# Kernel tuning notes

Measured on AMD Instinct MI355X. Metric: run time of the kernel, lower is better.

The kernel has to match this reference:

```python
import jax, jax.numpy as jnp
import numpy as np
import math

B, NI, NU, D, H, MAXNB, T = 1024, 50000, 20000, 256, 4, 20, 1000


def _cosine_sqrt_ab():
    t = jnp.linspace(0.0, T, T + 1) / T
    ab = jnp.cos((t + 0.008) / 1.008 * math.pi / 2) ** 2
    ab = ab / ab[0]
    ab = ab[1:]
    return jnp.sqrt(ab), jnp.sqrt(1.0 - ab)


def _ln(x, g, b, eps=1e-5):
    m = jnp.mean(x, -1, keepdims=True)
    v = jnp.var(x, -1, keepdims=True)
    return (x - m) / jnp.sqrt(v + eps) * g + b


def _mha(q, k, v, wqkv, bqkv, wo, bo):
    # torch nn.MultiheadAttention (batch_first) with packed in_proj
    d = q.shape[-1]
    dh = d // H
    wq, wk, wv = jnp.split(wqkv, 3, axis=0)
    bq, bk, bv = jnp.split(bqkv, 3, axis=0)
    def heads(x, w, bb):
        y = x @ w.T + bb
        return y.reshape(x.shape[0], x.shape[1], H, dh).transpose(0, 2, 1, 3)
    qh, kh, vh = heads(q, wq, bq), heads(k, wk, bk), heads(v, wv, bv)
    att = jax.nn.softmax(jnp.einsum('bhqd,bhkd->bhqk', qh, kh) / math.sqrt(dh), axis=-1)
    o = jnp.einsum('bhqk,bhkd->bhqd', att, vh)
    o = o.transpose(0, 2, 1, 3).reshape(q.shape[0], q.shape[1], d)
    return o @ wo.T + bo


def setup_inputs() -> dict:
    key = jax.random.key(0)
    ks = iter(jax.random.split(key, 64))
    p = lambda shape, s=0.02: jax.random.normal(next(ks), shape, jnp.float32) * s
    inp = {}
    inp['x0'] = (jax.random.uniform(next(ks), (B, NI)) < 0.05).astype(jnp.float32)
    inp['user_ids'] = jax.random.randint(next(ks), (B,), 0, NU)
    inp['t'] = jax.random.randint(next(ks), (B,), 0, T)
    inp['noise'] = jax.random.normal(next(ks), (B, D), jnp.float32)
    inp['neighbor_idx'] = jax.random.randint(next(ks), (NU, MAXNB), 0, NI)
    inp['item_emb'] = p((NI, D), 0.01)
    inp['enc_w1'] = p((2 * D, NI), 0.01); inp['enc_b1'] = jnp.zeros((2 * D,))
    inp['enc_w2'] = p((D, 2 * D)); inp['enc_b2'] = jnp.zeros((D,))
    inp['dec_w1'] = p((2 * D, D)); inp['dec_b1'] = jnp.zeros((2 * D,))
    inp['dec_w2'] = p((NI, 2 * D)); inp['dec_b2'] = jnp.zeros((NI,))
    inp['up_w'] = p((D, D)); inp['up_b'] = jnp.zeros((D,))
    inp['ip_w'] = p((D, D)); inp['ip_b'] = jnp.zeros((D,))
    inp['te_w1'] = p((32, 1)); inp['te_b1'] = jnp.zeros((32,))
    inp['te_w2'] = p((D, 32)); inp['te_b2'] = jnp.zeros((D,))
    inp['ca_wqkv'] = p((3 * D, D)); inp['ca_bqkv'] = jnp.zeros((3 * D,))
    inp['ca_wo'] = p((D, D)); inp['ca_bo'] = jnp.zeros((D,))
    inp['sa_wqkv'] = p((3 * D, D)); inp['sa_bqkv'] = jnp.zeros((3 * D,))
    inp['sa_wo'] = p((D, D)); inp['sa_bo'] = jnp.zeros((D,))
    inp['n1_g'] = jnp.ones((D,)); inp['n1_b'] = jnp.zeros((D,))
    inp['n2_g'] = jnp.ones((D,)); inp['n2_b'] = jnp.zeros((D,))
    inp['ff_w1'] = p((2 * D, D)); inp['ff_b1'] = jnp.zeros((2 * D,))
    inp['ff_w2'] = p((D, 2 * D)); inp['ff_b2'] = jnp.zeros((D,))
    return inp


def reference(x0, user_ids, t, noise, neighbor_idx, item_emb,
              enc_w1, enc_b1, enc_w2, enc_b2, dec_w1, dec_b1, dec_w2, dec_b2,
              up_w, up_b, ip_w, ip_b, te_w1, te_b1, te_w2, te_b2,
              ca_wqkv, ca_bqkv, ca_wo, ca_bo, sa_wqkv, sa_bqkv, sa_wo, sa_bo,
              n1_g, n1_b, n2_g, n2_b, ff_w1, ff_b1, ff_w2, ff_b2):
    gelu = lambda x: jax.nn.gelu(x, approximate=False)
    # encoder: (B, NI) -> (B, D)
    z0 = gelu(x0 @ enc_w1.T + enc_b1) @ enc_w2.T + enc_b2
    sqrt_ab, sqrt_1ab = _cosine_sqrt_ab()
    z_t = sqrt_ab[t][:, None] * z0 + sqrt_1ab[t][:, None] * noise
    # vectorized padded neighbor gather: (B, MAXNB, D)
    nb = item_emb[neighbor_idx[user_ids]]
    t_norm = t.astype(jnp.float32) / T
    # denoiser
    q = (z_t @ up_w.T + up_b)[:, None, :]
    kv = nb @ ip_w.T + ip_b
    te = jax.nn.silu(t_norm[:, None] @ te_w1.T + te_b1) @ te_w2.T + te_b2
    q = q + te[:, None, :]
    ca = _mha(q, kv, kv, ca_wqkv, ca_bqkv, ca_wo, ca_bo)
    h = _ln(q + ca, n1_g, n1_b)[:, 0, :]
    sa = _mha(h[:, None], h[:, None], h[:, None], sa_wqkv, sa_bqkv, sa_wo, sa_bo)[:, 0, :]
    h = _ln(h + sa, n2_g, n2_b)
    z_pred = h + (gelu(h @ ff_w1.T + ff_b1) @ ff_w2.T + ff_b2)
    diff_loss = jnp.mean((z_pred - z0) ** 2)
    logits = gelu(z0 @ dec_w1.T + dec_b1) @ dec_w2.T + dec_b2
    recon = jnp.mean(jax.nn.softplus(logits) - logits * x0)
    return diff_loss + 0.1 * recon
```

## Files before the change

### kernel.cpp

```cpp
#include <hip/hip_runtime.h>
#include <math.h>

#define NI   50000
#define Tt   1000
#define KP   50176
#define MW   1568
#define NPAD 50048

typedef __bf16 bf16x8 __attribute__((ext_vector_type(8)));
typedef float  f32x4  __attribute__((ext_vector_type(4)));

__device__ __forceinline__ unsigned short f2bf(float f) {
  unsigned u = __float_as_uint(f);
  u += 0x7FFFu + ((u >> 16) & 1u);
  return (unsigned short)(u >> 16);
}
__device__ __forceinline__ float bf2f(unsigned short u) {
  return __uint_as_float(((unsigned)u) << 16);
}
__device__ __forceinline__ unsigned pack2(float a, float b) {
  return (unsigned)f2bf(a) | ((unsigned)f2bf(b) << 16);
}
__device__ __forceinline__ f32x4 mfma16(const unsigned short* a, const unsigned short* b, f32x4 c) {
  typedef unsigned short u16x8 __attribute__((ext_vector_type(8)));
  u16x8 av = *(const u16x8*)a;
  u16x8 bv = *(const u16x8*)b;
  return __builtin_amdgcn_mfma_f32_16x16x32_bf16(
      __builtin_bit_cast(bf16x8, av), __builtin_bit_cast(bf16x8, bv), c, 0, 0, 0);
}
__device__ __forceinline__ float gelu_f(float x) {
  return 0.5f * x * (1.f + erff(x * 0.70710678118654752f));
}

#define GLD16(gsrc, ldst) __builtin_amdgcn_global_load_lds( \
    (const __attribute__((address_space(1))) unsigned int*)(const void*)(gsrc), \
    (__attribute__((address_space(3))) unsigned int*)(void*)(ldst), 16, 0, 0)
#define GLD4(gsrc, ldst) __builtin_amdgcn_global_load_lds( \
    (const __attribute__((address_space(1))) unsigned int*)(const void*)(gsrc), \
    (__attribute__((address_space(3))) unsigned int*)(void*)(ldst), 4, 0, 0)

#define PIPE_FENCE() __builtin_amdgcn_sched_barrier(0)
#define RAW_BAR()    __builtin_amdgcn_s_barrier()

#define MB_BM   25600
#define MB_W1   38400
#define MB_W2N  50900
#define MB_MANY 51348
#define MB_COMP 52116
#define MB_TE   53140

__global__ __launch_bounds__(256) void mega_prep(
    const float* __restrict__ x0, unsigned int* __restrict__ xmask,
    const float* __restrict__ enc_w1, unsigned short* __restrict__ w1b,
    const float* __restrict__ dec_w2, unsigned short* __restrict__ w2n,
    const float* s0, const float* s1, const float* s2, const float* s3,
    const float* s4, const float* s5, const float* s6,
    unsigned short* d0, unsigned short* d1, unsigned short* d2, unsigned short* d3,
    unsigned short* d4, unsigned short* d5, unsigned short* d6,
    const float* __restrict__ ca_wqkv, const float* __restrict__ ca_bqkv,
    const float* __restrict__ ip_w, const float* __restrict__ ip_b,
    const float* __restrict__ sa_wqkv, const float* __restrict__ sa_bqkv,
    const float* __restrict__ sa_wo, const float* __restrict__ sa_bo,
    unsigned short* __restrict__ Wkv, float* __restrict__ bkv,
    unsigned short* __restrict__ Wsa, float* __restrict__ bsa,
    const int* __restrict__ t,
    const float* __restrict__ te_w1, const float* __restrict__ te_b1,
    const float* __restrict__ te_w2, const float* __restrict__ te_b2,
    float* __restrict__ te, float* __restrict__ sab, float* __restrict__ s1ab)
{
  __shared__ unsigned int nib[256];
  __shared__ float sj[32];
  const int id = blockIdx.x, tid = threadIdx.x;

  if (id < MB_BM) {
    int r = id / 25, chunk = id % 25;
    int c0 = chunk * 2048;
    int k = c0 + tid * 8;
    const float* row = x0 + (size_t)r * NI;
    float4 a = make_float4(0.f, 0.f, 0.f, 0.f), b = a;
    if (k + 8 <= NI) {
      a = *(const float4*)(row + k);
      b = *(const float4*)(row + k + 4);
    }
    unsigned bits8 =
        (a.x != 0.f ? 1u : 0u)  | (a.y != 0.f ? 2u : 0u)  |
        (a.z != 0.f ? 4u : 0u)  | (a.w != 0.f ? 8u : 0u)  |
        (b.x != 0.f ? 16u : 0u) | (b.y != 0.f ? 32u : 0u) |
        (b.z != 0.f ? 64u : 0u) | (b.w != 0.f ? 128u : 0u);
    nib[tid] = bits8;
    __syncthreads();
    if (tid < 64) {
      unsigned wv = nib[tid * 4] | (nib[tid * 4 + 1] << 8) |
                    (nib[tid * 4 + 2] << 16) | (nib[tid * 4 + 3] << 24);
      int widx = (c0 >> 5) + tid;
      if (widx < MW) xmask[(size_t)r * MW + widx] = wv;
    }
  } else if (id < MB_W1) {
    int q = id - MB_BM;
    int r = q / 25, chunk = q % 25;
    int c = chunk * 2048 + tid * 8;
    if (c >= KP) return;
    const float* s = enc_w1 + (size_t)r * NI;
    uint4 o;
    if (c + 8 <= NI) {
      float4 a = *(const float4*)(s + c), b = *(const float4*)(s + c + 4);
      o.x = pack2(a.x, a.y); o.y = pack2(a.z, a.w);
      o.z = pack2(b.x, b.y); o.w = pack2(b.z, b.w);
    } else {
      float v[8];
#pragma unroll
      for (int i = 0; i < 8; ++i) v[i] = (c + i < NI) ? s[c + i] : 0.f;
      o.x = pack2(v[0], v[1]); o.y = pack2(v[2], v[3]);
      o.z = pack2(v[4], v[5]); o.w = pack2(v[6], v[7]);
    }
    *(uint4*)(w1b + (size_t)r * KP + c) = o;
  } else if (id < MB_W2N) {
    size_t idx = ((size_t)(id - MB_W1) * 256 + tid) * 8;
    float4 a = *(const float4*)(dec_w2 + idx), b = *(const float4*)(dec_w2 + idx + 4);
    uint4 o;
    o.x = pack2(a.x, a.y); o.y = pack2(a.z, a.w);
    o.z = pack2(b.x, b.y); o.w = pack2(b.z, b.w);
    *(uint4*)(w2n + idx) = o;
  } else if (id < MB_MANY) {
    const float* srcs[7] = {s0, s1, s2, s3, s4, s5, s6};
    unsigned short* dsts[7] = {d0, d1, d2, d3, d4, d5, d6};
    const int ns[7] = {131072, 65536, 65536, 65536, 131072, 131072, 131072};
    int q = id - MB_W2N;
    int j = q >> 6;
    int i = ((q & 63) * 256 + tid) * 8;
    if (i >= ns[j]) return;
    float4 a = *(const float4*)(srcs[j] + i), b = *(const float4*)(srcs[j] + i + 4);
    uint4 o;
    o.x = pack2(a.x, a.y); o.y = pack2(a.z, a.w);
    o.z = pack2(b.x, b.y); o.w = pack2(b.z, b.w);
    *(uint4*)(dsts[j] + i) = o;
  } else if (id < MB_COMP) {
    int b = id - MB_MANY, k = tid;
    if (b < 512) {
      const float* wrow = ca_wqkv + (size_t)(256 + b) * 256;
      float s = 0.f;
      for (int c = 0; c < 256; ++c) s += wrow[c] * ip_w[c * 256 + k];
      Wkv[b * 256 + k] = f2bf(s);
      if (k == 0) {
        float sb = 0.f;
        for (int c = 0; c < 256; ++c) sb += wrow[c] * ip_b[c];
        bkv[b] = sb + ca_bqkv[256 + b];
      }
    } else {
      int i = b - 512;
      const float* worow = sa_wo + (size_t)i * 256;
      float s = 0.f;
      for (int c = 0; c < 256; ++c) s += worow[c] * sa_wqkv[(512 + c) * 256 + k];
      Wsa[i * 256 + k] = f2bf(s);
      if (k == 0) {
        float sb = 0.f;
        for (int c = 0; c < 256; ++c) sb += worow[c] * sa_bqkv[512 + c];
        bsa[i] = sb + sa_bo[i];
      }
    }
  } else {
    int b = id - MB_COMP, d = tid;
    int ti = t[b];
    float tn = (float)ti / (float)Tt;
    if (d < 32) {
      float a = tn * te_w1[d] + te_b1[d];
      sj[d] = a / (1.f + __expf(-a));
    }
    if (d == 0) {
      double tt = (double)(ti + 1) / (double)Tt;
      double c  = cos((tt + 0.008) / 1.008 * M_PI * 0.5);
      double c0 = cos((0.008) / 1.008 * M_PI * 0.5);
      double ab = (c * c) / (c0 * c0);
      sab[b]  = (float)sqrt(ab);
      s1ab[b] = (float)sqrt(1.0 - ab);
    }
    __syncthreads();
    float accv = te_b2[d];
#pragma unroll
    for (int j = 0; j < 32; ++j) accv += sj[j] * te_w2[d * 32 + j];
    te[(size_t)b * 256 + d] = accv;
  }
}

__global__ __launch_bounds__(256) void enc_gemm(
    const unsigned int* __restrict__ xmask,
    const unsigned short* __restrict__ Bw,
    float* __restrict__ P0, float* __restrict__ P1)
{
  __shared__ __align__(16) unsigned short Bs[2][128 * 32];
  __shared__ __align__(16) unsigned short lut[256][8];
  __shared__ unsigned int mskb[2][4][64];
  const int tid = threadIdx.x;
  const int id = blockIdx.x;
  const int g = (id & 7) + 8 * (id >> 6);
  const int m0 = ((id >> 3) & 7) * 128;
  const int n0 = (g & 3) * 128;
  const int kc = g >> 2;
  const int kb = kc * 1568;
  const int w = tid >> 6, l = tid & 63;
  const int wm = (w >> 1) * 64, wn = (w & 1) * 64;
  const int fr = l & 15, fo = (l >> 4) * 8;
  const int s0 = tid, s1 = tid + 256;
  const unsigned short* Br0 = Bw + (size_t)(n0 + (s0 >> 2)) * KP + kb + (s0 & 3) * 8;
  const unsigned short* Br1 = Bw + (size_t)(n0 + (s1 >> 2)) * KP + kb + (s1 & 3) * 8;
  const unsigned int* msrc = xmask + (size_t)(m0 + wm + l) * MW + (kb >> 5);
  f32x4 acc[4][4] = {};

  {
    unsigned b = (unsigned)tid;
    uint4 q;
    q.x = (b & 1u   ? 0x3F80u : 0u) | (b & 2u   ? 0x3F800000u : 0u);
    q.y = (b & 4u   ? 0x3F80u : 0u) | (b & 8u   ? 0x3F800000u : 0u);
    q.z = (b & 16u  ? 0x3F80u : 0u) | (b & 32u  ? 0x3F800000u : 0u);
    q.w = (b & 64u  ? 0x3F80u : 0u) | (b & 128u ? 0x3F800000u : 0u);
    *(uint4*)&lut[tid][0] = q;
  }

#define STGE(IT, BUF) do {                                   \
    GLD4(msrc + (IT), &mskb[BUF][w][0]);                     \
    GLD16(Br0 + (IT) * 32, &Bs[BUF][s0 * 8]);                \
    GLD16(Br1 + (IT) * 32, &Bs[BUF][s1 * 8]); } while (0)

#define CMPE(BUF) do {                                                       \
    unsigned w0_ = mskb[BUF][w][fr];                                         \
    unsigned w1_ = mskb[BUF][w][16 + fr];                                    \
    unsigned w2_ = mskb[BUF][w][32 + fr];                                    \
    unsigned w3_ = mskb[BUF][w][48 + fr];                                    \
    const unsigned short* ap_[4];                                            \
    ap_[0] = &lut[(w0_ >> fo) & 0xFF][0];                                    \
    ap_[1] = &lut[(w1_ >> fo) & 0xFF][0];                                    \
    ap_[2] = &lut[(w2_ >> fo) & 0xFF][0];                                    \
    ap_[3] = &lut[(w3_ >> fo) & 0xFF][0];                                    \
    const unsigned short* bp_[4];                                            \
    _Pragma("unroll") for (int j_ = 0; j_ < 4; ++j_)                         \
      bp_[j_] = &Bs[BUF][(wn + 16 * j_ + fr) * 32 + fo];                     \
    _Pragma("unroll") for (int i_ = 0; i_ < 4; ++i_)                         \
    _Pragma("unroll") for (int j_ = 0; j_ < 4; ++j_)                         \
      acc[i_][j_] = mfma16(ap_[i_], bp_[j_], acc[i_][j_]); } while (0)

  STGE(0, 0);
  STGE(1, 1);
  asm volatile("s_waitcnt vmcnt(3) lgkmcnt(0)" ::: "memory");
  PIPE_FENCE(); RAW_BAR(); PIPE_FENCE();
  for (int it = 0; it < 49; ++it) {
    CMPE(it & 1);
    if (it == 48) break;
    PIPE_FENCE(); RAW_BAR(); PIPE_FENCE();
    if (it < 47) {
      STGE(it + 2, it & 1);
      asm volatile("s_waitcnt vmcnt(3) lgkmcnt(0)" ::: "memory");
    } else {
      asm volatile("s_waitcnt vmcnt(0) lgkmcnt(0)" ::: "memory");
    }
    PIPE_FENCE(); RAW_BAR(); PIPE_FENCE();
  }
#undef STGE
#undef CMPE

  const int cr = (l >> 4) * 4, cc = l & 15;
  float* Cp = ((kc < 16) ? P0 : P1) + (size_t)(kc & 15) * 524288;
#pragma unroll
  for (int i = 0; i < 4; ++i)
#pragma unroll
    for (int j = 0; j < 4; ++j) {
      int n = n0 + wn + 16 * j + cc;
#pragma unroll
      for (int r = 0; r < 4; ++r) {
        int m = m0 + wm + 16 * i + cr + r;
        Cp[(size_t)m * 512 + n] = acc[i][j][r];
      }
    }
}

template<int T>
__global__ __launch_bounds__(256) void gemm128(
    const unsigned short* __restrict__ A, int lda,
    const unsigned short* __restrict__ Bw, int ldb,
    const float* __restrict__ bias, void* __restrict__ Cv, int ldc, int K,
    const unsigned int* __restrict__ xmask, float* __restrict__ loss, int Nvalid)
{
  __shared__ __align__(16) unsigned short As[128 * 32];
  __shared__ __align__(16) unsigned short Bs[128 * 32];
  __shared__ unsigned int msk[128][4];
  __shared__ float red[4];
  const int tid = threadIdx.x;
  int m0, n0, iters;
  if (T == 1) {
    int id = blockIdx.x;
    int n = (id & 7) + 8 * (id >> 6);
    if (n >= 391) return;
    m0 = ((id >> 3) & 7) * 128;
    n0 = n * 128;
    iters = 16;
  } else {
    m0 = blockIdx.x * 128; n0 = blockIdx.y * 128;
    iters = K >> 5;
  }
  const int w = tid >> 6, l = tid & 63;
  const int wm = (w >> 1) * 64, wn = (w & 1) * 64;
  const int fr = l & 15, fo = (l >> 4) * 8;
  const int s0 = tid, s1 = tid + 256;
  f32x4 acc[4][4] = {};
  for (int it = 0; it < iters; ++it) {
    int k0 = it * 32;
    __syncthreads();
    GLD16(A  + (size_t)(m0 + (s0 >> 2)) * lda + k0 + (s0 & 3) * 8, &As[s0 * 8]);
    GLD16(A  + (size_t)(m0 + (s1 >> 2)) * lda + k0 + (s1 & 3) * 8, &As[s1 * 8]);
    GLD16(Bw + (size_t)(n0 + (s0 >> 2)) * ldb + k0 + (s0 & 3) * 8, &Bs[s0 * 8]);
    GLD16(Bw + (size_t)(n0 + (s1 >> 2)) * ldb + k0 + (s1 & 3) * 8, &Bs[s1 * 8]);
    __syncthreads();
    const unsigned short *ap[4], *bp[4];
#pragma unroll
    for (int i = 0; i < 4; ++i) {
      ap[i] = &As[(wm + 16 * i + fr) * 32 + fo];
      bp[i] = &Bs[(wn + 16 * i + fr) * 32 + fo];
    }
#pragma unroll
    for (int i = 0; i < 4; ++i)
#pragma unroll
      for (int j = 0; j < 4; ++j)
        acc[i][j] = mfma16(ap[i], bp[j], acc[i][j]);
  }
  const int cr = (l >> 4) * 4, cc = l & 15;
  if (T == 0) {
    unsigned short* Cb = (unsigned short*)Cv;
#pragma unroll
    for (int j = 0; j < 4; ++j) {
      int n = n0 + wn + 16 * j + cc;
      float bv = bias[n];
#pragma unroll
      for (int i = 0; i < 4; ++i)
#pragma unroll
        for (int r = 0; r < 4; ++r) {
          int m = m0 + wm + 16 * i + cr + r;
          Cb[(size_t)m * ldc + n] = f2bf(acc[i][j][r] + bv);
        }
    }
  } else {
    {
      int row = tid >> 1, p = tid & 1;
      *(uint2*)&msk[row][p * 2] =
          *(const uint2*)(xmask + (size_t)(m0 + row) * MW + (n0 >> 5) + p * 2);
    }
    __syncthreads();
    float ts = 0.f;
#pragma unroll
    for (int j = 0; j < 4; ++j) {
      int nl = wn + 16 * j + cc;
      int n = n0 + nl;
      if (n < Nvalid) {
        float bv = bias[n];
#pragma unroll
        for (int i = 0; i < 4; ++i)
#pragma unroll
          for (int r = 0; r < 4; ++r) {
            int ml = wm + 16 * i + cr + r;
            float lg = acc[i][j][r] + bv;
            float sp = fmaxf(lg, 0.f) + __logf(1.f + __expf(-fabsf(lg)));
            unsigned word = msk[ml][nl >> 5];
            ts += sp - (((word >> (nl & 31)) & 1u) ? lg : 0.f);
          }
      }
    }
    for (int off = 32; off > 0; off >>= 1) ts += __shfl_xor(ts, off);
    if (l == 0) red[w] = ts;
    __syncthreads();
    if (tid == 0) atomicAdd(loss, red[0] + red[1] + red[2] + red[3]);
  }
}

template<int EPI>
__global__ __launch_bounds__(256) void gemm64(
    const unsigned short* __restrict__ A, int lda,
    const unsigned short* __restrict__ Bw, int ldb,
    const float* __restrict__ bias, void* __restrict__ Cv, int ldc, int K,
    const void* __restrict__ R0, const void* __restrict__ R1, const void* __restrict__ R2,
    void* __restrict__ W0, void* __restrict__ W1, float* __restrict__ loss)
{
  __shared__ __align__(16) unsigned short As[64 * 32];
  __shared__ __align__(16) unsigned short Bs[64 * 32];
  __shared__ float red[4];
  const int tid = threadIdx.x;
  const int m0 = blockIdx.x * 64, n0 = blockIdx.y * 64;
  const int w = tid >> 6, l = tid & 63;
  const int wm = (w >> 1) * 32, wn = (w & 1) * 32;
  const int fr = l & 15, fo = (l >> 4) * 8;
  const int srow = tid >> 2, scol = (tid & 3) * 8;
  f32x4 acc[2][2] = {};
  for (int k0 = 0; k0 < K; k0 += 32) {
    __syncthreads();
    GLD16(A  + (size_t)(m0 + srow) * lda + k0 + scol, &As[tid * 8]);
    GLD16(Bw + (size_t)(n0 + srow) * ldb + k0 + scol, &Bs[tid * 8]);
    __syncthreads();
    const unsigned short* ap0 = &As[(wm +      fr) * 32 + fo];
    const unsigned short* ap1 = &As[(wm + 16 + fr) * 32 + fo];
    const unsigned short* bp0 = &Bs[(wn +      fr) * 32 + fo];
    const unsigned short* bp1 = &Bs[(wn + 16 + fr) * 32 + fo];
    acc[0][0] = mfma16(ap0, bp0, acc[0][0]);
    acc[0][1] = mfma16(ap0, bp1, acc[0][1]);
    acc[1][0] = mfma16(ap1, bp0, acc[1][0]);
    acc[1][1] = mfma16(ap1, bp1, acc[1][1]);
  }
  const int cr = (l >> 4) * 4, cc = l & 15;
  float ts = 0.f;
#pragma unroll
  for (int i = 0; i < 2; ++i)
#pragma unroll
    for (int j = 0; j < 2; ++j) {
      int n = n0 + wn + 16 * j + cc;
      float bv = bias[n];
#pragma unroll
      for (int r = 0; r < 4; ++r) {
        int m = m0 + wm + 16 * i + cr + r;
        float v = acc[i][j][r] + bv;
        size_t idx = (size_t)m * ldc + n;
        if (EPI == 0) ((float*)Cv)[idx] = v;
        if (EPI == 1) ((unsigned short*)Cv)[idx] = f2bf(v);
        if (EPI == 2) ((unsigned short*)Cv)[idx] = f2bf(gelu_f(v));
        if (EPI == 3) {
          ((float*)Cv)[idx] = v;
          ((unsigned short*)W0)[idx] = f2bf(v);
          float zt = ((const float*)R1)[m] * v +
                     ((const float*)R2)[m] * ((const float*)R0)[idx];
          ((unsigned short*)W1)[idx] = f2bf(zt);
        }
        if (EPI == 4) {
          v += ((const float*)R0)[idx];
          ((unsigned short*)Cv)[idx] = f2bf(v);
        }
        if (EPI == 5) {
          v += bf2f(((const unsigned short*)R0)[idx]);
          float d = v - ((const float*)R1)[idx];
          ts += d * d;
        }
      }
    }
  if (EPI == 5) {
    for (int off = 32; off > 0; off >>= 1) ts += __shfl_xor(ts, off);
    if (l == 0) red[w] = ts;
    __syncthreads();
    if (tid == 0) atomicAdd(loss, red[0] + red[1] + red[2] + red[3]);
  }
}

__global__ __launch_bounds__(256) void h1_epi(const float* __restrict__ P0,
                                              const float* __restrict__ P1,
                                              const float* __restrict__ b,
                                              unsigned short* __restrict__ H) {
  int i = blockIdx.x * 256 + threadIdx.x;
  float s = b[i & 511];
#pragma unroll
  for (int k = 0; k < 16; ++k) s += P0[(size_t)k * 524288 + i];
#pragma unroll
  for (int k = 0; k < 16; ++k) s += P1[(size_t)k * 524288 + i];
  H[i] = f2bf(gelu_f(s));
}

__global__ __launch_bounds__(256) void gather_nb(
    const int* __restrict__ uid, const int* __restrict__ nidx,
    const float* __restrict__ emb, unsigned short* __restrict__ nb)
{
  int b = blockIdx.x, j = blockIdx.y, d = threadIdx.x;
  int idx = nidx[uid[b] * 20 + j];
  nb[((size_t)b * 20 + j) * 256 + d] = f2bf(emb[(size_t)idx * 256 + d]);
}

__global__ __launch_bounds__(256) void attn_k(
    const float* __restrict__ qh, const unsigned short* __restrict__ kvh,
    unsigned short* __restrict__ o)
{
  int b = blockIdx.x, tid = threadIdx.x;
  int h = tid >> 6, d = tid & 63;
  float qv = qh[(size_t)b * 256 + h * 64 + d];
  const unsigned short* kbase = kvh + (size_t)b * 20 * 512 + h * 64 + d;
  const unsigned short* vbase = kbase + 256;
  float s[20];
#pragma unroll
  for (int k = 0; k < 20; ++k) {
    float p = qv * bf2f(kbase[k * 512]);
    for (int off = 32; off > 0; off >>= 1) p += __shfl_xor(p, off);
    s[k] = p * 0.125f;
  }
  float mx = s[0];
#pragma unroll
  for (int k = 1; k < 20; ++k) mx = fmaxf(mx, s[k]);
  float sum = 0.f;
#pragma unroll
  for (int k = 0; k < 20; ++k) { s[k] = __expf(s[k] - mx); sum += s[k]; }
  float inv = 1.f / sum;
  float ov = 0.f;
#pragma unroll
  for (int k = 0; k < 20; ++k) ov += s[k] * bf2f(vbase[k * 512]);
  o[(size_t)b * 256 + h * 64 + d] = f2bf(ov * inv);
}

__global__ __launch_bounds__(256) void ln_k(
    const unsigned short* __restrict__ X, const unsigned short* __restrict__ Y,
    const float* __restrict__ g, const float* __restrict__ bb,
    unsigned short* __restrict__ out)
{
  __shared__ float rs[4], rs2[4];
  int b = blockIdx.x, d = threadIdx.x;
  size_t i = (size_t)b * 256 + d;
  float v = bf2f(X[i]) + bf2f(Y[i]);
  float s = v, s2 = v * v;
  for (int off = 32; off > 0; off >>= 1) { s += __shfl_xor(s, off); s2 += __shfl_xor(s2, off); }
  int w = d >> 6, l = d & 63;
  if (l == 0) { rs[w] = s; rs2[w] = s2; }
  __syncthreads();
  s  = rs[0] + rs[1] + rs[2] + rs[3];
  s2 = rs2[0] + rs2[1] + rs2[2] + rs2[3];
  float mean = s * (1.f / 256.f);
  float var  = s2 * (1.f / 256.f) - mean * mean;
  out[i] = f2bf((v - mean) * rsqrtf(var + 1e-5f) * g[d] + bb[d]);
}

__global__ void final_k(const float* __restrict__ scal, float* __restrict__ out) {
  out[0] = scal[0] * (1.f / (1024.f * 256.f)) + 0.1f * scal[1] * (1.f / (1024.f * 50000.f));
}

extern "C" void kernel_launch(void* const* d_in, const int* in_sizes, int n_in,
                              void* d_out, int out_size, void* d_ws, size_t ws_size,
                              hipStream_t stream) {
  const float* x0      = (const float*)d_in[0];
  const int*   uid     = (const int*)  d_in[1];
  const int*   t       = (const int*)  d_in[2];
  const float* noise   = (const float*)d_in[3];
  const int*   nidx    = (const int*)  d_in[4];
  const float* item_emb= (const float*)d_in[5];
  const float* enc_w1  = (const float*)d_in[6];
  const float* enc_b1  = (const float*)d_in[7];
  const float* enc_w2  = (const float*)d_in[8];
  const float* enc_b2  = (const float*)d_in[9];
  const float* dec_w1  = (const float*)d_in[10];
  const float* dec_b1  = (const float*)d_in[11];
  const float* dec_w2  = (const float*)d_in[12];
  const float* dec_b2  = (const float*)d_in[13];
  const float* up_w    = (const float*)d_in[14];
  const float* up_b    = (const float*)d_in[15];
  const float* ip_w    = (const float*)d_in[16];
  const float* ip_b    = (const float*)d_in[17];
  const float* te_w1   = (const float*)d_in[18];
  const float* te_b1   = (const float*)d_in[19];
  const float* te_w2   = (const float*)d_in[20];
  const float* te_b2   = (const float*)d_in[21];
  const float* ca_wqkv = (const float*)d_in[22];
  const float* ca_bqkv = (const float*)d_in[23];
  const float* ca_wo   = (const float*)d_in[24];
  const float* ca_bo   = (const float*)d_in[25];
  const float* sa_wqkv = (const float*)d_in[26];
  const float* sa_bqkv = (const float*)d_in[27];
  const float* sa_wo   = (const float*)d_in[28];
  const float* sa_bo   = (const float*)d_in[29];
  const float* n1_g    = (const float*)d_in[30];
  const float* n1_b    = (const float*)d_in[31];
  const float* n2_g    = (const float*)d_in[32];
  const float* n2_b    = (const float*)d_in[33];
  const float* ff_w1   = (const float*)d_in[34];
  const float* ff_b1   = (const float*)d_in[35];
  const float* ff_w2   = (const float*)d_in[36];
  const float* ff_b2   = (const float*)d_in[37];
  (void)in_sizes; (void)n_in; (void)out_size; (void)ws_size;

  float* ws   = (float*)d_ws;
  float* scal = ws;
  float* sab  = ws + 4;
  float* s1ab = sab + 1024;
  float* te   = s1ab + 1024;
  float* qhf  = te + 262144;
  float* z0f  = qhf + 262144;
  float* bkv  = z0f + 262144;
  float* bsa  = bkv + 512;
  unsigned int* xmask = (unsigned int*)(bsa + 256);
  unsigned short* sh  = (unsigned short*)(xmask + 1024 * MW);
  float*          OUTp = (float*)sh;
  unsigned short* nbb  = sh;
  unsigned short* kvhb = nbb + 5242880;
  unsigned short* f1b  = kvhb + 10485760;
  unsigned short* Gb   = f1b + 524288;
  unsigned short* x0b  = Gb + 524288;
  unsigned short* w2n  = x0b;
  unsigned short* w1b  = x0b + (size_t)1024 * KP;
  unsigned short* H1b  = w1b + (size_t)512 * KP;
  unsigned short* z0b  = H1b + 524288;
  unsigned short* ztb  = z0b + 262144;
  unsigned short* qpb  = ztb + 262144;
  unsigned short* ob   = qpb + 262144;
  unsigned short* cab  = ob  + 262144;
  unsigned short* hb   = cab + 262144;
  unsigned short* saob = hb  + 262144;
  unsigned short* h2b  = saob+ 262144;
  unsigned short* enc_w2b = h2b + 262144;
  unsigned short* up_wb   = enc_w2b + 131072;
  unsigned short* ca_wqb  = up_wb + 65536;
  unsigned short* ca_wob  = ca_wqb + 65536;
  unsigned short* ff_w1b  = ca_wob + 65536;
  unsigned short* ff_w2b  = ff_w1b + 131072;
  unsigned short* dec_w1b = ff_w2b + 131072;
  unsigned short* Wkv     = dec_w1b + 131072;
  unsigned short* Wsab    = Wkv + 131072;
  float*          OUTp2   = (float*)(Wsab + 131072);

  hipMemsetAsync(scal, 0, 4 * sizeof(float), stream);

  mega_prep<<<MB_TE, 256, 0, stream>>>(
      x0, xmask, enc_w1, w1b, dec_w2, w2n,
      enc_w2, up_w, ca_wqkv, ca_wo, ff_w1, ff_w2, dec_w1,
      enc_w2b, up_wb, ca_wqb, ca_wob, ff_w1b, ff_w2b, dec_w1b,
      ca_wqkv, ca_bqkv, ip_w, ip_b, sa_wqkv, sa_bqkv, sa_wo, sa_bo,
      Wkv, bkv, Wsab, bsa,
      t, te_w1, te_b1, te_w2, te_b2, te, sab, s1ab);

  enc_gemm<<<1024, 256, 0, stream>>>(xmask, w1b, OUTp, OUTp2);
  h1_epi<<<2048, 256, 0, stream>>>(OUTp, OUTp2, enc_b1, H1b);

  gather_nb<<<dim3(1024, 20), 256, 0, stream>>>(uid, nidx, item_emb, nbb);
  gemm128<0><<<dim3(160, 4), 256, 0, stream>>>(
      nbb, 256, Wkv, 256, bkv, kvhb, 512, 256, nullptr, nullptr, 0);

  gemm64<3><<<dim3(16, 4), 256, 0, stream>>>(
      H1b, 512, enc_w2b, 512, enc_b2, z0f, 256, 512, noise, sab, s1ab, z0b, ztb, nullptr);

  gemm64<4><<<dim3(16, 4), 256, 0, stream>>>(
      ztb, 256, up_wb, 256, up_b, qpb, 256, 256, te, nullptr, nullptr, nullptr, nullptr, nullptr);
  gemm64<0><<<dim3(16, 4), 256, 0, stream>>>(
      qpb, 256, ca_wqb, 256, ca_bqkv, qhf, 256, 256,
      nullptr, nullptr, nullptr, nullptr, nullptr, nullptr);

  attn_k<<<1024, 256, 0, stream>>>(qhf, kvhb, ob);
  gemm64<1><<<dim3(16, 4), 256, 0, stream>>>(
      ob, 256, ca_wob, 256, ca_bo, cab, 256, 256,
      nullptr, nullptr, nullptr, nullptr, nullptr, nullptr);
  ln_k<<<1024, 256, 0, stream>>>(qpb, cab, n1_g, n1_b, hb);

  gemm64<1><<<dim3(16, 4), 256, 0, stream>>>(
      hb, 256, Wsab, 256, bsa, saob, 256, 256,
      nullptr, nullptr, nullptr, nullptr, nullptr, nullptr);
  ln_k<<<1024, 256, 0, stream>>>(hb, saob, n2_g, n2_b, h2b);

  gemm64<2><<<dim3(16, 8), 256, 0, stream>>>(
      h2b, 256, ff_w1b, 256, ff_b1, f1b, 512, 256,
      nullptr, nullptr, nullptr, nullptr, nullptr, nullptr);
  gemm64<5><<<dim3(16, 4), 256, 0, stream>>>(
      f1b, 512, ff_w2b, 512, ff_b2, nullptr, 256, 512,
      h2b, z0f, nullptr, nullptr, nullptr, &scal[0]);

  gemm64<2><<<dim3(16, 8), 256, 0, stream>>>(
      z0b, 256, dec_w1b, 256, dec_b1, Gb, 512, 256,
      nullptr, nullptr, nullptr, nullptr, nullptr, nullptr);
  gemm128<1><<<3136, 256, 0, stream>>>(
      Gb, 512, w2n, 512, dec_b2, nullptr, 0, 512, xmask, &scal[1], NI);

  final_k<<<1, 1, 0, stream>>>(scal, (float*)d_out);
}
```

Measured before the change: 855.6 us.

## Split prep into critical path and overlap remaining prep with encoder GEMM

The monolithic prep kernel is split. A small critical kernel builds the x0 bitmask, now also in a transposed word-major layout, and converts enc_w1 to bf16. The encoder GEMM then runs fused in one launch with the remaining prep work (dec_w2 conversion, small weight casts, composed weights, time embedding), so that bandwidth-heavy conversion overlaps MFMA compute. The GEMM k-loop is restructured to process two 32-wide k-slices per barrier using the transposed mask for coalesced loads. The neighbor gather also uses one block per batch row instead of one per (row, neighbor). The risks are contention between the co-resident conversion blocks and the GEMM, and the extra xmaskT write.

```diff
diff --git a/kernel.cpp b/kernel.cpp
--- a/kernel.cpp
+++ b/kernel.cpp
@@ -42,21 +42,94 @@
 #define PIPE_FENCE() __builtin_amdgcn_sched_barrier(0)
 #define RAW_BAR()    __builtin_amdgcn_s_barrier()
 
-#define MB_BM   25600
-#define MB_W1   38400
-#define MB_W2N  50900
-#define MB_MANY 51348
-#define MB_COMP 52116
-#define MB_TE   53140
-
-__global__ __launch_bounds__(256) void mega_prep(
+__global__ __launch_bounds__(256) void prep_crit(
     const float* __restrict__ x0, unsigned int* __restrict__ xmask,
-    const float* __restrict__ enc_w1, unsigned short* __restrict__ w1b,
+    unsigned int* __restrict__ xmaskT,
+    const float* __restrict__ enc_w1, unsigned short* __restrict__ w1b)
+{
+  __shared__ unsigned int T[32][64];
+  __shared__ unsigned int nib[256];
+  const int id = blockIdx.x, tid = threadIdx.x;
+  if (id < 800) {
+    int rg = id / 25, ch = id % 25;
+    int r0 = rg * 32, c0 = ch * 2048, c0w = ch * 64;
+    for (int rr = 0; rr < 32; ++rr) {
+      int k = c0 + tid * 8;
+      const float* row = x0 + (size_t)(r0 + rr) * NI;
+      float4 a = make_float4(0.f, 0.f, 0.f, 0.f), b = a;
+      if (k + 8 <= NI) {
+        a = *(const float4*)(row + k);
+        b = *(const float4*)(row + k + 4);
+      }
+      unsigned bits8 =
+          (a.x != 0.f ? 1u : 0u)  | (a.y != 0.f ? 2u : 0u)  |
+          (a.z != 0.f ? 4u : 0u)  | (a.w != 0.f ? 8u : 0u)  |
+          (b.x != 0.f ? 16u : 0u) | (b.y != 0.f ? 32u : 0u) |
+          (b.z != 0.f ? 64u : 0u) | (b.w != 0.f ? 128u : 0u);
+      nib[tid] = bits8;
+      __syncthreads();
+      if (tid < 64) {
+        T[rr][tid] = nib[tid * 4] | (nib[tid * 4 + 1] << 8) |
+                     (nib[tid * 4 + 2] << 16) | (nib[tid * 4 + 3] << 24);
+      }
+      __syncthreads();
+    }
+    {
+      int rr = tid >> 3, wg = (tid & 7) * 8;
+      if (c0w + wg < MW) {
+        unsigned* dst = xmask + (size_t)(r0 + rr) * MW + c0w + wg;
+        uint4 q0 = make_uint4(T[rr][wg], T[rr][wg+1], T[rr][wg+2], T[rr][wg+3]);
+        uint4 q1 = make_uint4(T[rr][wg+4], T[rr][wg+5], T[rr][wg+6], T[rr][wg+7]);
+        *(uint4*)dst = q0; *(uint4*)(dst + 4) = q1;
+      }
+    }
+    {
+      int ww = tid >> 2, rg8 = (tid & 3) * 8;
+      if (c0w + ww < MW) {
+        unsigned* dst = xmaskT + (size_t)(c0w + ww) * 1024 + r0 + rg8;
+        uint4 q0 = make_uint4(T[rg8][ww], T[rg8+1][ww], T[rg8+2][ww], T[rg8+3][ww]);
+        uint4 q1 = make_uint4(T[rg8+4][ww], T[rg8+5][ww], T[rg8+6][ww], T[rg8+7][ww]);
+        *(uint4*)dst = q0; *(uint4*)(dst + 4) = q1;
+      }
+    }
+  } else {
+    int r = id - 800;
+    const float* s = enc_w1 + (size_t)r * NI;
+    for (int ch = 0; ch < 25; ++ch) {
+      int c = ch * 2048 + tid * 8;
+      if (c >= KP) continue;
+      uint4 o;
+      if (c + 8 <= NI) {
+        float4 a = *(const float4*)(s + c), b = *(const float4*)(s + c + 4);
+        o.x = pack2(a.x, a.y); o.y = pack2(a.z, a.w);
+        o.z = pack2(b.x, b.y); o.w = pack2(b.z, b.w);
+      } else {
+        float v[8];
+#pragma unroll
+        for (int i = 0; i < 8; ++i) v[i] = (c + i < NI) ? s[c + i] : 0.f;
+        o.x = pack2(v[0], v[1]); o.y = pack2(v[2], v[3]);
+        o.z = pack2(v[4], v[5]); o.w = pack2(v[6], v[7]);
+      }
+      *(uint4*)(w1b + (size_t)r * KP + c) = o;
+    }
+  }
+}
+
+#define EF_ENC  1024
+#define EF_W2N  2592
+#define EF_MANY 3040
+#define EF_COMP 3808
+#define EF_TE   4832
+
+__global__ __launch_bounds__(256) void enc_fused(
+    const unsigned int* __restrict__ xmaskT,
+    const unsigned short* __restrict__ Bw,
+    float* __restrict__ P0, float* __restrict__ P1,
     const float* __restrict__ dec_w2, unsigned short* __restrict__ w2n,
-    const float* s0, const float* s1, const float* s2, const float* s3,
-    const float* s4, const float* s5, const float* s6,
-    unsigned short* d0, unsigned short* d1, unsigned short* d2, unsigned short* d3,
-    unsigned short* d4, unsigned short* d5, unsigned short* d6,
+    const float* s0a, const float* s1a, const float* s2a, const float* s3a,
+    const float* s4a, const float* s5a, const float* s6a,
+    unsigned short* d0a, unsigned short* d1a, unsigned short* d2a, unsigned short* d3a,
+    unsigned short* d4a, unsigned short* d5a, unsigned short* d6a,
     const float* __restrict__ ca_wqkv, const float* __restrict__ ca_bqkv,
     const float* __restrict__ ip_w, const float* __restrict__ ip_b,
     const float* __restrict__ sa_wqkv, const float* __restrict__ sa_bqkv,
@@ -68,64 +141,113 @@
     const float* __restrict__ te_w2, const float* __restrict__ te_b2,
     float* __restrict__ te, float* __restrict__ sab, float* __restrict__ s1ab)
 {
-  __shared__ unsigned int nib[256];
+  __shared__ __align__(16) unsigned short BsE[2][2][128 * 32];
+  __shared__ __align__(16) unsigned short lut[256][8];
+  __shared__ unsigned int mskb[2][2][128];
   __shared__ float sj[32];
   const int id = blockIdx.x, tid = threadIdx.x;
 
-  if (id < MB_BM) {
-    int r = id / 25, chunk = id % 25;
-    int c0 = chunk * 2048;
-    int k = c0 + tid * 8;
-    const float* row = x0 + (size_t)r * NI;
-    float4 a = make_float4(0.f, 0.f, 0.f, 0.f), b = a;
-    if (k + 8 <= NI) {
-      a = *(const float4*)(row + k);
-      b = *(const float4*)(row + k + 4);
-    }
-    unsigned bits8 =
-        (a.x != 0.f ? 1u : 0u)  | (a.y != 0.f ? 2u : 0u)  |
-        (a.z != 0.f ? 4u : 0u)  | (a.w != 0.f ? 8u : 0u)  |
-        (b.x != 0.f ? 16u : 0u) | (b.y != 0.f ? 32u : 0u) |
-        (b.z != 0.f ? 64u : 0u) | (b.w != 0.f ? 128u : 0u);
-    nib[tid] = bits8;
-    __syncthreads();
-    if (tid < 64) {
-      unsigned wv = nib[tid * 4] | (nib[tid * 4 + 1] << 8) |
-                    (nib[tid * 4 + 2] << 16) | (nib[tid * 4 + 3] << 24);
-      int widx = (c0 >> 5) + tid;
-      if (widx < MW) xmask[(size_t)r * MW + widx] = wv;
-    }
-  } else if (id < MB_W1) {
-    int q = id - MB_BM;
-    int r = q / 25, chunk = q % 25;
-    int c = chunk * 2048 + tid * 8;
-    if (c >= KP) return;
-    const float* s = enc_w1 + (size_t)r * NI;
-    uint4 o;
-    if (c + 8 <= NI) {
-      float4 a = *(const float4*)(s + c), b = *(const float4*)(s + c + 4);
+  if (id < EF_ENC) {
+    const int g = (id & 7) + 8 * (id >> 6);
+    const int m0 = ((id >> 3) & 7) * 128;
+    const int n0 = (g & 3) * 128;
+    const int kc = g >> 2;
+    const int kb = kc * 1568;
+    const int kw0 = kc * 49;
+    const int w = tid >> 6, l = tid & 63;
+    const int wm = (w >> 1) * 64, wn = (w & 1) * 64;
+    const int fr = l & 15, fo = (l >> 4) * 8;
+    const int s0 = tid, s1 = tid + 256;
+    const unsigned short* Br0 = Bw + (size_t)(n0 + (s0 >> 2)) * KP + kb + (s0 & 3) * 8;
+    const unsigned short* Br1 = Bw + (size_t)(n0 + (s1 >> 2)) * KP + kb + (s1 & 3) * 8;
+    f32x4 acc[4][4] = {};
+
+    {
+      unsigned b = (unsigned)tid;
+      uint4 q;
+      q.x = (b & 1u   ? 0x3F80u : 0u) | (b & 2u   ? 0x3F800000u : 0u);
+      q.y = (b & 4u   ? 0x3F80u : 0u) | (b & 8u   ? 0x3F800000u : 0u);
+      q.z = (b & 16u  ? 0x3F80u : 0u) | (b & 32u  ? 0x3F800000u : 0u);
+      q.w = (b & 64u  ? 0x3F80u : 0u) | (b & 128u ? 0x3F800000u : 0u);
+      *(uint4*)&lut[tid][0] = q;
+    }
+
+#define STGF(IT, BUF) do {                                                  \
+    GLD4(xmaskT + (size_t)(kw0 + (IT) * 2 + (w & 1)) * 1024                 \
+                + m0 + (w >> 1) * 64 + l,                                   \
+         &mskb[BUF][w & 1][(w >> 1) * 64]);                                 \
+    GLD16(Br0 + (IT) * 64,      &BsE[BUF][0][s0 * 8]);                      \
+    GLD16(Br1 + (IT) * 64,      &BsE[BUF][0][s1 * 8]);                      \
+    GLD16(Br0 + (IT) * 64 + 32, &BsE[BUF][1][s0 * 8]);                      \
+    GLD16(Br1 + (IT) * 64 + 32, &BsE[BUF][1][s1 * 8]); } while (0)
+
+#define STGT(BUF) do {                                                      \
+    GLD4(xmaskT + (size_t)(kw0 + 48) * 1024 + m0 + (w & 1) * 64 + l,        \
+         &mskb[BUF][0][(w & 1) * 64]);                                      \
+    GLD16(Br0 + 24 * 64, &BsE[BUF][0][s0 * 8]);                             \
+    GLD16(Br1 + 24 * 64, &BsE[BUF][0][s1 * 8]); } while (0)
+
+#define CMPH(BUF, KK) do {                                                  \
+    const unsigned short *ap_[4], *bp_[4];                                  \
+    _Pragma("unroll") for (int i_ = 0; i_ < 4; ++i_)                        \
+      ap_[i_] = &lut[(mskb[BUF][KK][wm + 16 * i_ + fr] >> fo) & 0xFF][0];   \
+    _Pragma("unroll") for (int j_ = 0; j_ < 4; ++j_)                        \
+      bp_[j_] = &BsE[BUF][KK][(wn + 16 * j_ + fr) * 32 + fo];               \
+    _Pragma("unroll") for (int i_ = 0; i_ < 4; ++i_)                        \
+    _Pragma("unroll") for (int j_ = 0; j_ < 4; ++j_)                        \
+      acc[i_][j_] = mfma16(ap_[i_], bp_[j_], acc[i_][j_]); } while (0)
+
+    STGF(0, 0);
+    STGF(1, 1);
+    asm volatile("s_waitcnt vmcnt(5) lgkmcnt(0)" ::: "memory");
+    PIPE_FENCE(); RAW_BAR(); PIPE_FENCE();
+    for (int it = 0; it < 24; ++it) {
+      CMPH(it & 1, 0);
+      CMPH(it & 1, 1);
+      PIPE_FENCE(); RAW_BAR(); PIPE_FENCE();
+      if (it < 22) {
+        STGF(it + 2, it & 1);
+        asm volatile("s_waitcnt vmcnt(5)" ::: "memory");
+      } else if (it == 22) {
+        STGT(0);
+        asm volatile("s_waitcnt vmcnt(3)" ::: "memory");
+      } else {
+        asm volatile("s_waitcnt vmcnt(0)" ::: "memory");
+      }
+      PIPE_FENCE(); RAW_BAR(); PIPE_FENCE();
+    }
+    CMPH(0, 0);
+#undef STGF
+#undef STGT
+#undef CMPH
+
+    const int cr = (l >> 4) * 4, cc = l & 15;
+    float* Cp = ((kc < 16) ? P0 : P1) + (size_t)(kc & 15) * 524288;
+#pragma unroll
+    for (int i = 0; i < 4; ++i)
+#pragma unroll
+      for (int j = 0; j < 4; ++j) {
+        int n = n0 + wn + 16 * j + cc;
+#pragma unroll
+        for (int r = 0; r < 4; ++r) {
+          int m = m0 + wm + 16 * i + cr + r;
+          Cp[(size_t)m * 512 + n] = acc[i][j][r];
+        }
+      }
+  } else if (id < EF_W2N) {
+    size_t b2 = id - EF_ENC;
+    for (size_t e = (b2 * 256 + tid) * 8; e < 25600000u; e += (size_t)1568 * 256 * 8) {
+      float4 a = *(const float4*)(dec_w2 + e), b = *(const float4*)(dec_w2 + e + 4);
+      uint4 o;
       o.x = pack2(a.x, a.y); o.y = pack2(a.z, a.w);
       o.z = pack2(b.x, b.y); o.w = pack2(b.z, b.w);
-    } else {
-      float v[8];
-#pragma unroll
-      for (int i = 0; i < 8; ++i) v[i] = (c + i < NI) ? s[c + i] : 0.f;
-      o.x = pack2(v[0], v[1]); o.y = pack2(v[2], v[3]);
-      o.z = pack2(v[4], v[5]); o.w = pack2(v[6], v[7]);
-    }
-    *(uint4*)(w1b + (size_t)r * KP + c) = o;
-  } else if (id < MB_W2N) {
-    size_t idx = ((size_t)(id - MB_W1) * 256 + tid) * 8;
-    float4 a = *(const float4*)(dec_w2 + idx), b = *(const float4*)(dec_w2 + idx + 4);
-    uint4 o;
-    o.x = pack2(a.x, a.y); o.y = pack2(a.z, a.w);
-    o.z = pack2(b.x, b.y); o.w = pack2(b.z, b.w);
-    *(uint4*)(w2n + idx) = o;
-  } else if (id < MB_MANY) {
-    const float* srcs[7] = {s0, s1, s2, s3, s4, s5, s6};
-    unsigned short* dsts[7] = {d0, d1, d2, d3, d4, d5, d6};
+      *(uint4*)(w2n + e) = o;
+    }
+  } else if (id < EF_MANY) {
+    const float* srcs[7] = {s0a, s1a, s2a, s3a, s4a, s5a, s6a};
+    unsigned short* dsts[7] = {d0a, d1a, d2a, d3a, d4a, d5a, d6a};
     const int ns[7] = {131072, 65536, 65536, 65536, 131072, 131072, 131072};
-    int q = id - MB_W2N;
+    int q = id - EF_W2N;
     int j = q >> 6;
     int i = ((q & 63) * 256 + tid) * 8;
     if (i >= ns[j]) return;
@@ -134,8 +256,8 @@
     o.x = pack2(a.x, a.y); o.y = pack2(a.z, a.w);
     o.z = pack2(b.x, b.y); o.w = pack2(b.z, b.w);
     *(uint4*)(dsts[j] + i) = o;
-  } else if (id < MB_COMP) {
-    int b = id - MB_MANY, k = tid;
+  } else if (id < EF_COMP) {
+    int b = id - EF_MANY, k = tid;
     if (b < 512) {
       const float* wrow = ca_wqkv + (size_t)(256 + b) * 256;
       float s = 0.f;
@@ -159,7 +281,7 @@
       }
     }
   } else {
-    int b = id - MB_COMP, d = tid;
+    int b = id - EF_COMP, d = tid;
     int ti = t[b];
     float tn = (float)ti / (float)Tt;
     if (d < 32) {
@@ -180,96 +302,6 @@
     for (int j = 0; j < 32; ++j) accv += sj[j] * te_w2[d * 32 + j];
     te[(size_t)b * 256 + d] = accv;
   }
-}
-
-__global__ __launch_bounds__(256) void enc_gemm(
-    const unsigned int* __restrict__ xmask,
-    const unsigned short* __restrict__ Bw,
-    float* __restrict__ P0, float* __restrict__ P1)
-{
-  __shared__ __align__(16) unsigned short Bs[2][128 * 32];
-  __shared__ __align__(16) unsigned short lut[256][8];
-  __shared__ unsigned int mskb[2][4][64];
-  const int tid = threadIdx.x;
-  const int id = blockIdx.x;
-  const int g = (id & 7) + 8 * (id >> 6);
-  const int m0 = ((id >> 3) & 7) * 128;
-  const int n0 = (g & 3) * 128;
-  const int kc = g >> 2;
-  const int kb = kc * 1568;
-  const int w = tid >> 6, l = tid & 63;
-  const int wm = (w >> 1) * 64, wn = (w & 1) * 64;
-  const int fr = l & 15, fo = (l >> 4) * 8;
-  const int s0 = tid, s1 = tid + 256;
-  const unsigned short* Br0 = Bw + (size_t)(n0 + (s0 >> 2)) * KP + kb + (s0 & 3) * 8;
-  const unsigned short* Br1 = Bw + (size_t)(n0 + (s1 >> 2)) * KP + kb + (s1 & 3) * 8;
-  const unsigned int* msrc = xmask + (size_t)(m0 + wm + l) * MW + (kb >> 5);
-  f32x4 acc[4][4] = {};
-
-  {
-    unsigned b = (unsigned)tid;
-    uint4 q;
-    q.x = (b & 1u   ? 0x3F80u : 0u) | (b & 2u   ? 0x3F800000u : 0u);
-    q.y = (b & 4u   ? 0x3F80u : 0u) | (b & 8u   ? 0x3F800000u : 0u);
-    q.z = (b & 16u  ? 0x3F80u : 0u) | (b & 32u  ? 0x3F800000u : 0u);
-    q.w = (b & 64u  ? 0x3F80u : 0u) | (b & 128u ? 0x3F800000u : 0u);
-    *(uint4*)&lut[tid][0] = q;
-  }
-
-#define STGE(IT, BUF) do {                                   \
-    GLD4(msrc + (IT), &mskb[BUF][w][0]);                     \
-    GLD16(Br0 + (IT) * 32, &Bs[BUF][s0 * 8]);                \
-    GLD16(Br1 + (IT) * 32, &Bs[BUF][s1 * 8]); } while (0)
-
-#define CMPE(BUF) do {                                                       \
-    unsigned w0_ = mskb[BUF][w][fr];                                         \
-    unsigned w1_ = mskb[BUF][w][16 + fr];                                    \
-    unsigned w2_ = mskb[BUF][w][32 + fr];                                    \
-    unsigned w3_ = mskb[BUF][w][48 + fr];                                    \
-    const unsigned short* ap_[4];                                            \
-    ap_[0] = &lut[(w0_ >> fo) & 0xFF][0];                                    \
-    ap_[1] = &lut[(w1_ >> fo) & 0xFF][0];                                    \
-    ap_[2] = &lut[(w2_ >> fo) & 0xFF][0];                                    \
-    ap_[3] = &lut[(w3_ >> fo) & 0xFF][0];                                    \
-    const unsigned short* bp_[4];                                            \
-    _Pragma("unroll") for (int j_ = 0; j_ < 4; ++j_)                         \
-      bp_[j_] = &Bs[BUF][(wn + 16 * j_ + fr) * 32 + fo];                     \
-    _Pragma("unroll") for (int i_ = 0; i_ < 4; ++i_)                         \
-    _Pragma("unroll") for (int j_ = 0; j_ < 4; ++j_)                         \
-      acc[i_][j_] = mfma16(ap_[i_], bp_[j_], acc[i_][j_]); } while (0)
-
-  STGE(0, 0);
-  STGE(1, 1);
-  asm volatile("s_waitcnt vmcnt(3) lgkmcnt(0)" ::: "memory");
-  PIPE_FENCE(); RAW_BAR(); PIPE_FENCE();
-  for (int it = 0; it < 49; ++it) {
-    CMPE(it & 1);
-    if (it == 48) break;
-    PIPE_FENCE(); RAW_BAR(); PIPE_FENCE();
-    if (it < 47) {
-      STGE(it + 2, it & 1);
-      asm volatile("s_waitcnt vmcnt(3) lgkmcnt(0)" ::: "memory");
-    } else {
-      asm volatile("s_waitcnt vmcnt(0) lgkmcnt(0)" ::: "memory");
-    }
-    PIPE_FENCE(); RAW_BAR(); PIPE_FENCE();
-  }
-#undef STGE
-#undef CMPE
-
-  const int cr = (l >> 4) * 4, cc = l & 15;
-  float* Cp = ((kc < 16) ? P0 : P1) + (size_t)(kc & 15) * 524288;
-#pragma unroll
-  for (int i = 0; i < 4; ++i)
-#pragma unroll
-    for (int j = 0; j < 4; ++j) {
-      int n = n0 + wn + 16 * j + cc;
-#pragma unroll
-      for (int r = 0; r < 4; ++r) {
-        int m = m0 + wm + 16 * i + cr + r;
-        Cp[(size_t)m * 512 + n] = acc[i][j][r];
-      }
-    }
 }
 
 template<int T>
@@ -460,9 +492,13 @@
     const int* __restrict__ uid, const int* __restrict__ nidx,
     const float* __restrict__ emb, unsigned short* __restrict__ nb)
 {
-  int b = blockIdx.x, j = blockIdx.y, d = threadIdx.x;
-  int idx = nidx[uid[b] * 20 + j];
-  nb[((size_t)b * 20 + j) * 256 + d] = f2bf(emb[(size_t)idx * 256 + d]);
+  int b = blockIdx.x, d = threadIdx.x;
+  const int* np = nidx + uid[b] * 20;
+#pragma unroll
+  for (int j = 0; j < 20; ++j) {
+    int idx = np[j];
+    nb[((size_t)b * 20 + j) * 256 + d] = f2bf(emb[(size_t)idx * 256 + d]);
+  }
 }
 
 __global__ __launch_bounds__(256) void attn_k(
@@ -580,6 +616,7 @@
   unsigned short* Gb   = f1b + 524288;
   unsigned short* x0b  = Gb + 524288;
   unsigned short* w2n  = x0b;
+  unsigned int*   xmaskT = (unsigned int*)(x0b + 26214400);
   unsigned short* w1b  = x0b + (size_t)1024 * KP;
   unsigned short* H1b  = w1b + (size_t)512 * KP;
   unsigned short* z0b  = H1b + 524288;
@@ -603,18 +640,19 @@
 
   hipMemsetAsync(scal, 0, 4 * sizeof(float), stream);
 
-  mega_prep<<<MB_TE, 256, 0, stream>>>(
-      x0, xmask, enc_w1, w1b, dec_w2, w2n,
+  prep_crit<<<1312, 256, 0, stream>>>(x0, xmask, xmaskT, enc_w1, w1b);
+
+  enc_fused<<<EF_TE, 256, 0, stream>>>(
+      xmaskT, w1b, OUTp, OUTp2,
+      dec_w2, w2n,
       enc_w2, up_w, ca_wqkv, ca_wo, ff_w1, ff_w2, dec_w1,
       enc_w2b, up_wb, ca_wqb, ca_wob, ff_w1b, ff_w2b, dec_w1b,
       ca_wqkv, ca_bqkv, ip_w, ip_b, sa_wqkv, sa_bqkv, sa_wo, sa_bo,
       Wkv, bkv, Wsab, bsa,
       t, te_w1, te_b1, te_w2, te_b2, te, sab, s1ab);
-
-  enc_gemm<<<1024, 256, 0, stream>>>(xmask, w1b, OUTp, OUTp2);
   h1_epi<<<2048, 256, 0, stream>>>(OUTp, OUTp2, enc_b1, H1b);
 
-  gather_nb<<<dim3(1024, 20), 256, 0, stream>>>(uid, nidx, item_emb, nbb);
+  gather_nb<<<1024, 256, 0, stream>>>(uid, nidx, item_emb, nbb);
   gemm128<0><<<dim3(160, 4), 256, 0, stream>>>(
       nbb, 256, Wkv, 256, bkv, kvhb, 512, 256, nullptr, nullptr, 0);
 
```

Measured after the change: 827.7 us. -3.3%, faster.
